# Optimization experiments

Measured on AMD Instinct MI355X. Metric: run time of the kernel, lower is better.

## Reference

```python
import jax, jax.numpy as jnp
import numpy as np

EPS = 1e-5

def group_norm(x, num_groups, eps=EPS):
    # x: [B, C, H, W]; no affine (matches F.group_norm with weight=None)
    B, C, H, W = x.shape
    xg = x.reshape(B, num_groups, (C // num_groups) * H * W)
    mean = jnp.mean(xg, axis=-1, keepdims=True)
    var = jnp.var(xg, axis=-1, keepdims=True)
    xg = (xg - mean) * jax.lax.rsqrt(var + eps)
    return xg.reshape(B, C, H, W)

def setup_inputs() -> dict:
    key = jax.random.key(0)
    ks = jax.random.split(key, 5)
    B, C, H, W = 32, 256, 32, 32
    # kaiming-uniform-ish scale for linear weights
    bound = 1.0 / np.sqrt(C)
    x = jax.random.normal(ks[0], (B, C, H, W), dtype=jnp.float32)
    WQ = jax.random.uniform(ks[1], (C, C), jnp.float32, -bound, bound)
    WK = jax.random.uniform(ks[2], (C, C), jnp.float32, -bound, bound)
    WV = jax.random.uniform(ks[3], (C, C), jnp.float32, -bound, bound)
    Wo = jax.random.uniform(ks[4], (C, C), jnp.float32, -bound, bound)
    z = jnp.zeros((C,), jnp.float32)
    return {"x": x, "WQ": WQ, "bQ": z, "WK": WK, "bK": z,
            "WV": WV, "bV": z, "Wo": Wo, "bo": z}

def reference(x, WQ, bQ, WK, bK, WV, bV, Wo, bo):
    B, C, H, W = x.shape
    G = min(32, C)
    h = group_norm(x, G)                      # [B,C,H,W]
    h = h.reshape(B, C, H * W).transpose(0, 2, 1)  # [B, S, C], S = H*W
    q = h @ WQ + bQ
    k = h @ WK + bK
    v = h @ WV + bV
    scale = C ** (-0.5)
    attn = jnp.einsum('bsc,btc->bst', q, k) * scale   # [B,S,S]
    attn = jax.nn.softmax(attn, axis=-1)
    o = jnp.einsum('bst,btc->bsc', attn, v)           # [B,S,C]
    o = o @ Wo + bo                                   # output Nin while in [B,S,C]
    o = o.transpose(0, 2, 1).reshape(B, C, H, W)
    return x + o
```

## Files before the change

kernel.cpp:

```cpp
#include <hip/hip_runtime.h>
#include <stdint.h>

#define BB  32
#define CC  256
#define SS  1024
#define GG  32
#define GCH 8
#define EPS 1e-5f

typedef __attribute__((ext_vector_type(8))) short short8;
typedef __attribute__((ext_vector_type(4))) float f32x4;
typedef unsigned short ushort;

__device__ __forceinline__ float bf2f(ushort u){
  union { unsigned int i; float f; } v; v.i = ((unsigned int)u) << 16; return v.f;
}
__device__ __forceinline__ ushort f2bf(float f){
  union { float f; unsigned int i; } v; v.f = f;
  unsigned int r = v.i + 0x7FFFu + ((v.i >> 16) & 1u);
  return (ushort)(r >> 16);
}

typedef __attribute__((address_space(3))) unsigned int lds_uint;
typedef const __attribute__((address_space(1))) unsigned int glob_uint;
__device__ __forceinline__ void ld_lds16(const void* g, void* l){
  __builtin_amdgcn_global_load_lds((glob_uint*)g, (lds_uint*)l, 16, 0, 0);
}

__global__ __launch_bounds__(256) void sniff_k(const unsigned int* __restrict__ xw,
                                               int* __restrict__ flag)
{
  const int tid = threadIdx.x;
  unsigned int w = xw[tid];
  ushort lo = (ushort)(w & 0xFFFFu);
  int e = (lo >> 7) & 0xFF;
  int ok = (lo == 0 || (e >= 100 && e <= 130)) ? 1 : 0;
  __shared__ int cnt;
  if (tid == 0) cnt = 0;
  __syncthreads();
  atomicAdd(&cnt, ok);
  __syncthreads();
  if (tid == 0) *flag = (cnt > 192) ? 1 : 0;
}

__global__ __launch_bounds__(256) void convert_pre(
    const void* w0, const void* w1, const void* w2, const void* w3,
    const void* b0, const void* b1, const void* b2, const void* b3,
    ushort* __restrict__ WT, float* __restrict__ biasF,
    const int* __restrict__ flag)
{
  const int f = *flag;
  const int z = blockIdx.z;
  const float scl = (z == 0) ? 0.0625f : 1.0f;
  const void* wsel = z==0?w0:z==1?w1:z==2?w2:w3;
  ushort* dst = WT + (long long)z * 65536;
  __shared__ ushort t[64][65];
  const int tid = threadIdx.x;
  const int tx = tid & 63, ty = tid >> 6;
  const int r0 = blockIdx.x * 64, c0 = blockIdx.y * 64;
  for (int j = 0; j < 64; j += 4){
    const int idx = (r0+ty+j)*256 + c0+tx;
    float v = f ? bf2f(((const ushort*)wsel)[idx]) : ((const float*)wsel)[idx];
    t[ty+j][tx] = f2bf(v * scl);
  }
  __syncthreads();
  for (int j = 0; j < 64; j += 4) dst[(c0+ty+j)*256 + r0+tx] = t[tx][ty+j];
  if (blockIdx.x == 0 && blockIdx.y == 0){
    const void* bsel = z==0?b0:z==1?b1:z==2?b2:b3;
    float bv = f ? bf2f(((const ushort*)bsel)[tid]) : ((const float*)bsel)[tid];
    biasF[z*256 + tid] = bv * scl;
  }
}

__global__ __launch_bounds__(256) void gn_stats(const void* __restrict__ x,
                                                float* __restrict__ stats,
                                                const int* __restrict__ flag)
{
  const int f = *flag;
  const int g = blockIdx.x, b = blockIdx.y;
  const int tid = threadIdx.x;
  const long long base = ((long long)b * CC + g * GCH) * SS;
  float sum = 0.f, ss = 0.f;
  if (f){
    const ushort* xg = (const ushort*)x + base;
    #pragma unroll
    for (int j = 0; j < 4; j++){
      uint4 u = *(const uint4*)(xg + (j*256 + tid)*8);
      const ushort* e = (const ushort*)&u;
      #pragma unroll
      for (int i = 0; i < 8; i++){ float v = bf2f(e[i]); sum += v; ss += v*v; }
    }
  } else {
    const float* xg = (const float*)x + base;
    #pragma unroll
    for (int j = 0; j < 8; j++){
      float4 v4 = *(const float4*)(xg + (j*256 + tid)*4);
      sum += v4.x+v4.y+v4.z+v4.w;
      ss  += v4.x*v4.x+v4.y*v4.y+v4.z*v4.z+v4.w*v4.w;
    }
  }
  __shared__ float red[8];
  const int lane = tid & 63, w = tid >> 6;
  #pragma unroll
  for (int o = 32; o > 0; o >>= 1){
    sum += __shfl_down(sum, o);
    ss  += __shfl_down(ss, o);
  }
  if (lane == 0){ red[w] = sum; red[4+w] = ss; }
  __syncthreads();
  if (tid == 0){
    float s1 = red[0]+red[1]+red[2]+red[3];
    float s2 = red[4]+red[5]+red[6]+red[7];
    float mean = s1 / (float)(GCH*SS);
    float var  = s2 / (float)(GCH*SS) - mean*mean;
    const int idx = b*GG + g;
    stats[idx*2]   = mean;
    stats[idx*2+1] = rsqrtf(var + EPS);
  }
}

__global__ __launch_bounds__(256) void gn_norm(const void* __restrict__ x,
                                               ushort* __restrict__ h,
                                               const float* __restrict__ stats,
                                               const int* __restrict__ flag)
{
  const int f = *flag;
  const int c0 = blockIdx.x * 64, s0 = blockIdx.y * 64, b = blockIdx.z;
  const int tid = threadIdx.x;
  __shared__ ushort T[64][72];
  const int row = tid >> 2;
  const int qr  = tid & 3;
  const int g = (c0 + row) >> 3;
  const float mean = stats[(b*GG + g)*2];
  const float rstd = stats[(b*GG + g)*2 + 1];
  const long long xrow = ((long long)b * CC + c0 + row) * SS + s0;
  if (f){
    const ushort* xr = (const ushort*)x + xrow;
    #pragma unroll
    for (int j = 0; j < 2; j++){
      const int col = qr*16 + j*8;
      uint4 u = *(const uint4*)(xr + col);
      const ushort* e = (const ushort*)&u;
      #pragma unroll
      for (int i = 0; i < 8; i++) T[row][col+i] = f2bf((bf2f(e[i]) - mean) * rstd);
    }
  } else {
    const float* xr = (const float*)x + xrow;
    #pragma unroll
    for (int j = 0; j < 4; j++){
      const int col = qr*16 + j*4;
      float4 v4 = *(const float4*)(xr + col);
      T[row][col+0] = f2bf((v4.x - mean) * rstd);
      T[row][col+1] = f2bf((v4.y - mean) * rstd);
      T[row][col+2] = f2bf((v4.z - mean) * rstd);
      T[row][col+3] = f2bf((v4.w - mean) * rstd);
    }
  }
  __syncthreads();
  #pragma unroll
  for (int pass = 0; pass < 2; pass++){
    const int sr = pass*32 + (tid >> 3);
    const int cl = (tid & 7) * 8;
    ushort tmp[8];
    #pragma unroll
    for (int e = 0; e < 8; e++) tmp[e] = T[cl+e][sr];
    *(uint4*)(&h[((long long)b * SS + s0 + sr) * CC + c0 + cl]) = *(const uint4*)tmp;
  }
}

template<int MODE>
__global__ __launch_bounds__(256) void gemm128(
    const ushort* __restrict__ A,
    const ushort* __restrict__ BT,
    ushort* __restrict__ Cmat,
    int lda, int ldb, int ldc, int K,
    long long sA, long long sB, long long sC,
    const float* __restrict__ biasF,
    const void* __restrict__ xres,
    void* __restrict__ outp,
    ushort* __restrict__ vTp,
    long long xoff,
    const int* __restrict__ flag)
{
  extern __shared__ __attribute__((aligned(16))) ushort smem[];
  ushort* As = smem;
  ushort* Bs = smem + 5120;
  const int tid  = threadIdx.x;
  const int lane = tid & 63;
  const int w    = tid >> 6;
  const int wr   = w >> 1, wc = w & 1;
  const int bz   = blockIdx.z;
  const int m0 = blockIdx.x * 128;
  const int n0 = blockIdx.y * 128;

  const int srow  = tid >> 1;
  const int shalf = (tid & 1) * 16;

  f32x4 acc[4][4] = {};

  const ushort* Ablk = A + (long long)bz * sA + (long long)(m0 + srow) * lda + shalf;
  const ushort* Bblk = BT + (long long)bz * sB + (long long)(n0 + srow) * ldb + shalf;
  ushort* asw = &As[srow * 40 + shalf];
  ushort* bsw = &Bs[srow * 40 + shalf];

  const int koff = 8 * (lane >> 4);
  const int rr   = lane & 15;

  for (int k0 = 0; k0 < K; k0 += 32){
    uint4 va0 = *(const uint4*)(Ablk + k0);
    uint4 va1 = *(const uint4*)(Ablk + k0 + 8);
    uint4 vb0 = *(const uint4*)(Bblk + k0);
    uint4 vb1 = *(const uint4*)(Bblk + k0 + 8);
    *(uint4*)(asw)     = va0;
    *(uint4*)(asw + 8) = va1;
    *(uint4*)(bsw)     = vb0;
    *(uint4*)(bsw + 8) = vb1;
    __syncthreads();
    short8 af[4], bfr[4];
    #pragma unroll
    for (int mf = 0; mf < 4; mf++)
      af[mf] = *(const short8*)(&As[(wr*64 + mf*16 + rr) * 40 + koff]);
    #pragma unroll
    for (int nf = 0; nf < 4; nf++)
      bfr[nf] = *(const short8*)(&Bs[(wc*64 + nf*16 + rr) * 40 + koff]);
    #pragma unroll
    for (int mf = 0; mf < 4; mf++)
      #pragma unroll
      for (int nf = 0; nf < 4; nf++)
        acc[mf][nf] = __builtin_amdgcn_mfma_f32_16x16x32_bf16(af[mf], bfr[nf], acc[mf][nf], 0, 0, 0);
    __syncthreads();
  }

  const int rb = 4 * (lane >> 4);
  if (MODE == 0){
    if (bz < 2){
      ushort* Co = Cmat + (long long)bz * sC;
      #pragma unroll
      for (int mf = 0; mf < 4; mf++){
        #pragma unroll
        for (int nf = 0; nf < 4; nf++){
          const int col = n0 + wc*64 + nf*16 + rr;
          const float badd = biasF[bz*256 + col];
          #pragma unroll
          for (int r = 0; r < 4; r++){
            const int row = m0 + wr*64 + mf*16 + rb + r;
            Co[(long long)row * ldc + col] = f2bf(acc[mf][nf][r] + badd);
          }
        }
      }
    } else {
      #pragma unroll
      for (int mf = 0; mf < 4; mf++){
        #pragma unroll
        for (int nf = 0; nf < 4; nf++){
          const int col = n0 + wc*64 + nf*16 + rr;
          const float badd = biasF[512 + col];
          #pragma unroll
          for (int r = 0; r < 4; r++){
            const int row = m0 + wr*64 + mf*16 + rb + r;
            const int bL = row >> 10, s = row & 1023;
            vTp[((long long)bL * CC + col) * SS + s] = f2bf(acc[mf][nf][r] + badd);
          }
        }
      }
    }
  } else {
    const int bL = m0 >> 10;
    const int s0 = m0 & 1023;
    #pragma unroll
    for (int mf = 0; mf < 4; mf++){
      #pragma unroll
      for (int nf = 0; nf < 4; nf++){
        const int colL = wc*64 + nf*16 + rr;
        const float badd = biasF[768 + n0 + colL];
        #pragma unroll
        for (int r = 0; r < 4; r++){
          const int rowL = wr*64 + mf*16 + rb + r;
          smem[colL * 128 + rowL] = f2bf(acc[mf][nf][r] + badd);
        }
      }
    }
    __syncthreads();
    const int f = *flag;
    for (int i = tid; i < 2048; i += 256){
      const int colL = i >> 4;
      const int rowL = (i & 15) * 8;
      const long long oi = xoff + ((long long)bL * CC + n0 + colL) * SS + s0 + rowL;
      const ushort* pu = &smem[colL * 128 + rowL];
      if (f){
        const ushort* xu = (const ushort*)xres + oi;
        ushort* ou = (ushort*)outp + oi;
        ushort tmp[8];
        #pragma unroll
        for (int e = 0; e < 8; e++) tmp[e] = f2bf(bf2f(xu[e]) + bf2f(pu[e]));
        *(uint4*)ou = *(const uint4*)tmp;
      } else {
        const float* xf = (const float*)xres + oi;
        float* of = (float*)outp + oi;
        float4 a0 = *(const float4*)xf;
        float4 a1 = *(const float4*)(xf + 4);
        float4 r0, r1;
        r0.x = a0.x + bf2f(pu[0]); r0.y = a0.y + bf2f(pu[1]);
        r0.z = a0.z + bf2f(pu[2]); r0.w = a0.w + bf2f(pu[3]);
        r1.x = a1.x + bf2f(pu[4]); r1.y = a1.y + bf2f(pu[5]);
        r1.z = a1.z + bf2f(pu[6]); r1.w = a1.w + bf2f(pu[7]);
        *(float4*)of = r0;
        *(float4*)(of + 4) = r1;
      }
    }
  }
}

__global__ __launch_bounds__(256, 2) void attn_fused(
    const ushort* __restrict__ q, const ushort* __restrict__ k,
    const ushort* __restrict__ vT, ushort* __restrict__ oC)
{
  __shared__ ushort Kb[64 * 256];
  __shared__ ushort Vb[256 * 64];
  __shared__ ushort Pb[64 * 64];
  const int tid = threadIdx.x, lane = tid & 63, w = tid >> 6;
  const int hi = lane >> 4, rr = lane & 15;
  const int b = blockIdx.x, qt = blockIdx.y;

  const ushort* qg = q + ((long long)b * SS + qt * 64) * CC;
  const char* kgB = (const char*)(k + (long long)b * SS * CC);
  const char* vgB = (const char*)(vT + (long long)b * CC * SS);
  ushort* og = oC + ((long long)b * SS + qt * 64) * CC;

  short8 qf[8];
  #pragma unroll
  for (int ks = 0; ks < 8; ks++)
    qf[ks] = *(const short8*)(qg + (w*16 + rr) * CC + ks*32 + 8*hi);

  f32x4 Oa[16] = {};
  float mrow[4], lrow[4];
  #pragma unroll
  for (int r = 0; r < 4; r++){ mrow[r] = -1e30f; lrow[r] = 0.0f; }

  for (int t0 = 0; t0 < SS; t0 += 64){
    #pragma unroll
    for (int j = 0; j < 8; j++){
      const int tr = j*8 + w*2 + (lane >> 5);
      const int xb = ((lane & 31) * 16) ^ ((tr & 7) << 4);
      ld_lds16(kgB + (long long)(t0 + tr) * 512 + xb, &Kb[(j*8 + w*2) * 256]);
    }
    #pragma unroll
    for (int j = 0; j < 8; j++){
      const int c0 = (j*4 + w) * 8;
      const int cr = c0 + (lane >> 3);
      const int yb = ((lane & 7) * 16) ^ ((cr & 7) << 4);
      ld_lds16(vgB + (long long)cr * 2048 + t0*2 + yb, &Vb[c0 * 64]);
    }
    asm volatile("s_waitcnt vmcnt(0)" ::: "memory");
    __builtin_amdgcn_sched_barrier(0);
    __syncthreads();

    f32x4 Sa[4] = {};
    __builtin_amdgcn_s_setprio(1);
    #pragma unroll
    for (int ks = 0; ks < 8; ks++){
      short8 bk[4];
      #pragma unroll
      for (int nf = 0; nf < 4; nf++){
        const int t = nf*16 + rr;
        const int byte = t*512 + ((ks*64 + hi*16) ^ ((t & 7) << 4));
        bk[nf] = *(const short8*)((const char*)Kb + byte);
      }
      #pragma unroll
      for (int nf = 0; nf < 4; nf++)
        Sa[nf] = __builtin_amdgcn_mfma_f32_16x16x32_bf16(qf[ks], bk[nf], Sa[nf], 0, 0, 0);
    }
    __builtin_amdgcn_s_setprio(0);

    #pragma unroll
    for (int r = 0; r < 4; r++){
      float pm = fmaxf(fmaxf(Sa[0][r], Sa[1][r]), fmaxf(Sa[2][r], Sa[3][r]));
      pm = fmaxf(pm, __shfl_xor(pm, 1));
      pm = fmaxf(pm, __shfl_xor(pm, 2));
      pm = fmaxf(pm, __shfl_xor(pm, 4));
      pm = fmaxf(pm, __shfl_xor(pm, 8));
      const float mo = mrow[r];
      const float mn = fmaxf(mo, pm);
      const float sc = __expf(mo - mn);
      float ps[4];
      #pragma unroll
      for (int nf = 0; nf < 4; nf++) ps[nf] = __expf(Sa[nf][r] - mn);
      float rs = ps[0] + ps[1] + ps[2] + ps[3];
      rs += __shfl_xor(rs, 1);
      rs += __shfl_xor(rs, 2);
      rs += __shfl_xor(rs, 4);
      rs += __shfl_xor(rs, 8);
      lrow[r] = lrow[r] * sc + rs;
      mrow[r] = mn;
      const int qloc = w*16 + 4*hi + r;
      const int swz = (qloc & 7) << 4;
      #pragma unroll
      for (int nf = 0; nf < 4; nf++){
        const int byte = qloc*128 + ((2*(nf*16 + rr)) ^ swz);
        *(ushort*)((char*)Pb + byte) = f2bf(ps[nf]);
      }
      #pragma unroll
      for (int nf2 = 0; nf2 < 16; nf2++) Oa[nf2][r] *= sc;
    }

    __builtin_amdgcn_s_setprio(1);
    #pragma unroll
    for (int ks2 = 0; ks2 < 2; ks2++){
      const int qloc = w*16 + rr;
      const int pbyte = qloc*128 + ((ks2*64 + 16*hi) ^ ((qloc & 7) << 4));
      short8 pa = *(const short8*)((const char*)Pb + pbyte);
      #pragma unroll
      for (int nf = 0; nf < 16; nf++){
        const int c = nf*16 + rr;
        const int byte = c*128 + ((ks2*64 + 16*hi) ^ ((c & 7) << 4));
        short8 bv = *(const short8*)((const char*)Vb + byte);
        Oa[nf] = __builtin_amdgcn_mfma_f32_16x16x32_bf16(pa, bv, Oa[nf], 0, 0, 0);
      }
    }
    __builtin_amdgcn_s_setprio(0);
    __syncthreads();
  }

  #pragma unroll
  for (int r = 0; r < 4; r++){
    const float inv = 1.0f / lrow[r];
    const int qloc = w*16 + 4*hi + r;
    #pragma unroll
    for (int nf = 0; nf < 16; nf++)
      og[(long long)qloc * CC + nf*16 + rr] = f2bf(Oa[nf][r] * inv);
  }
}

extern "C" void kernel_launch(void* const* d_in, const int* in_sizes, int n_in,
                              void* d_out, int out_size, void* d_ws, size_t ws_size,
                              hipStream_t stream)
{
  (void)in_sizes; (void)n_in; (void)out_size;
  const void* x  = d_in[0];
  const void* WQ = d_in[1];
  const void* bQ = d_in[2];
  const void* WK = d_in[3];
  const void* bK = d_in[4];
  const void* WV = d_in[5];
  const void* bV = d_in[6];
  const void* Wo = d_in[7];
  const void* bo = d_in[8];

  const long long NE  = (long long)BB * SS * CC;
  const long long SC  = (long long)SS * CC;

  uint8_t* base = (uint8_t*)d_ws;
  int* flag          = (int*)base;
  float* biasF       = (float*)(base + 256);
  float* stats       = (float*)(base + 256 + 4096);
  ushort* WT         = (ushort*)(base + 256 + 4096 + 8192);
  ushort* h          = WT + 4 * 65536;

  const long long fixedB = 256 + 4096 + 8192 + 4LL*65536*2 + NE*2;
  int CB = 1;
  for (int c = 32; c >= 1; c >>= 1){
    if (fixedB + 4LL * c * SC * 2 <= (long long)ws_size){ CB = c; break; }
  }

  ushort* q  = h + NE;
  ushort* k  = q + (long long)CB * SC;
  ushort* vT = k + (long long)CB * SC;
  ushort* oC = vT + (long long)CB * SC;

  dim3 blk(256);
  const size_t shmem = 32768;

  sniff_k<<<1, blk, 0, stream>>>((const unsigned int*)x, flag);
  convert_pre<<<dim3(4, 4, 4), blk, 0, stream>>>(WQ, WK, WV, Wo, bQ, bK, bV, bo, WT, biasF, flag);
  gn_stats<<<dim3(GG, BB), blk, 0, stream>>>(x, stats, flag);
  gn_norm<<<dim3(4, 16, BB), blk, 0, stream>>>(x, h, stats, flag);

  for (int c0 = 0; c0 < BB; c0 += CB){
    const ushort* hC = h + (long long)c0 * SC;
    gemm128<0><<<dim3(CB*8, 2, 3), blk, shmem, stream>>>(
        hC, WT, q, CC, CC, CC, CC,
        0LL, 65536LL, (long long)CB * SC,
        biasF, nullptr, nullptr, vT, 0LL, flag);
    attn_fused<<<dim3(CB, 16), blk, 0, stream>>>(q, k, vT, oC);
    gemm128<3><<<dim3(CB*8, 2, 1), blk, shmem, stream>>>(
        oC, WT + 3*65536, nullptr, CC, CC, SS, CC,
        0LL, 0LL, 0LL,
        biasF, x, d_out, nullptr, (long long)c0 * SC, flag);
  }
}
```

Before: 148.2 us.

## Rewrite attention kernel with 32x32 MFMA and direct global K/V loads

```diff
diff --git a/kernel.cpp b/kernel.cpp
--- a/kernel.cpp
+++ b/kernel.cpp
@@ -10,6 +10,7 @@
 
 typedef __attribute__((ext_vector_type(8))) short short8;
 typedef __attribute__((ext_vector_type(4))) float f32x4;
+typedef __attribute__((ext_vector_type(16))) float f32x16;
 typedef unsigned short ushort;
 
 __device__ __forceinline__ float bf2f(ushort u){
@@ -19,12 +20,6 @@
   union { float f; unsigned int i; } v; v.f = f;
   unsigned int r = v.i + 0x7FFFu + ((v.i >> 16) & 1u);
   return (ushort)(r >> 16);
-}
-
-typedef __attribute__((address_space(3))) unsigned int lds_uint;
-typedef const __attribute__((address_space(1))) unsigned int glob_uint;
-__device__ __forceinline__ void ld_lds16(const void* g, void* l){
-  __builtin_amdgcn_global_load_lds((glob_uint*)g, (lds_uint*)l, 16, 0, 0);
 }
 
 __global__ __launch_bounds__(256) void sniff_k(const unsigned int* __restrict__ xw,
@@ -315,119 +310,112 @@
     const ushort* __restrict__ q, const ushort* __restrict__ k,
     const ushort* __restrict__ vT, ushort* __restrict__ oC)
 {
-  __shared__ ushort Kb[64 * 256];
-  __shared__ ushort Vb[256 * 64];
-  __shared__ ushort Pb[64 * 64];
+  __shared__ ushort Pall[4][2048];
+  __shared__ float  Sall[4][32];
   const int tid = threadIdx.x, lane = tid & 63, w = tid >> 6;
-  const int hi = lane >> 4, rr = lane & 15;
-  const int b = blockIdx.x, qt = blockIdx.y;
-
-  const ushort* qg = q + ((long long)b * SS + qt * 64) * CC;
-  const char* kgB = (const char*)(k + (long long)b * SS * CC);
-  const char* vgB = (const char*)(vT + (long long)b * CC * SS);
-  ushort* og = oC + ((long long)b * SS + qt * 64) * CC;
-
-  short8 qf[8];
+  const int l31 = lane & 31, hi2 = lane >> 5;
+  const int qh = w & 1, ch = w >> 1;
+  const int qt = blockIdx.x, b = blockIdx.y;
+
+  const ushort* qg = q + ((long long)b * SS + qt*64 + qh*32 + l31) * CC + 8*hi2;
+  const ushort* kbase = k + (long long)b * SS * CC + (long long)l31 * CC + 8*hi2;
+  const ushort* vbase = vT + (long long)b * CC * SS + (long long)(ch*128 + l31) * SS + 8*hi2;
+  ushort* og = oC + ((long long)b * SS + qt*64 + qh*32) * CC + ch*128;
+
+  char* PwB = (char*)&Pall[w][0];
+  float* Sw = &Sall[w][0];
+  const int swz = (l31 & 7) << 4;
+
+  short8 qf[16];
   #pragma unroll
-  for (int ks = 0; ks < 8; ks++)
-    qf[ks] = *(const short8*)(qg + (w*16 + rr) * CC + ks*32 + 8*hi);
-
-  f32x4 Oa[16] = {};
-  float mrow[4], lrow[4];
+  for (int kk = 0; kk < 16; kk++)
+    qf[kk] = *(const short8*)(qg + kk*16);
+
+  f32x16 Oa[4] = {};
+  float mrow = -1e30f, lrow = 0.0f;
+
+  for (int t0 = 0; t0 < SS; t0 += 64){
+    const ushort* kt0 = kbase + (long long)t0 * CC;
+    const ushort* kt1 = kt0 + 32 * CC;
+
+    f32x16 Sa0 = {}, Sa1 = {};
+    __builtin_amdgcn_s_setprio(1);
+    #pragma unroll
+    for (int kk = 0; kk < 16; kk++){
+      short8 ka0 = *(const short8*)(kt0 + kk*16);
+      short8 ka1 = *(const short8*)(kt1 + kk*16);
+      Sa0 = __builtin_amdgcn_mfma_f32_32x32x16_bf16(ka0, qf[kk], Sa0, 0, 0, 0);
+      Sa1 = __builtin_amdgcn_mfma_f32_32x32x16_bf16(ka1, qf[kk], Sa1, 0, 0, 0);
+    }
+    __builtin_amdgcn_s_setprio(0);
+
+    float mx = -1e30f;
+    #pragma unroll
+    for (int r = 0; r < 16; r++){ mx = fmaxf(mx, Sa0[r]); mx = fmaxf(mx, Sa1[r]); }
+    mx = fmaxf(mx, __shfl_xor(mx, 32));
+    const float mn = fmaxf(mrow, mx);
+    const float sc = __expf(mrow - mn);
+    mrow = mn;
+    float rs = 0.0f;
+    #pragma unroll
+    for (int r = 0; r < 16; r++){
+      Sa0[r] = __expf(Sa0[r] - mn); rs += Sa0[r];
+      Sa1[r] = __expf(Sa1[r] - mn); rs += Sa1[r];
+    }
+    rs += __shfl_xor(rs, 32);
+    lrow = lrow * sc + rs;
+
+    if (hi2 == 0) Sw[l31] = sc;
+
+    #pragma unroll
+    for (int g2 = 0; g2 < 4; g2++){
+      ushort t4[4];
+      #pragma unroll
+      for (int j = 0; j < 4; j++) t4[j] = f2bf(Sa0[g2*4 + j]);
+      *(uint2*)(PwB + l31*128 + ((g2*16 + hi2*8) ^ swz)) = *(const uint2*)t4;
+      #pragma unroll
+      for (int j = 0; j < 4; j++) t4[j] = f2bf(Sa1[g2*4 + j]);
+      *(uint2*)(PwB + l31*128 + ((64 + g2*16 + hi2*8) ^ swz)) = *(const uint2*)t4;
+    }
+
+    f32x4 scv[4];
+    #pragma unroll
+    for (int g2 = 0; g2 < 4; g2++)
+      scv[g2] = *(const f32x4*)((const char*)Sw + g2*32 + hi2*16);
+    #pragma unroll
+    for (int nf = 0; nf < 4; nf++)
+      #pragma unroll
+      for (int r = 0; r < 16; r++)
+        Oa[nf][r] *= scv[r >> 2][r & 3];
+
+    __builtin_amdgcn_s_setprio(1);
+    #pragma unroll
+    for (int kk = 0; kk < 4; kk++){
+      short8 pa = *(const short8*)(PwB + l31*128 + ((kk*32 + hi2*16) ^ swz));
+      #pragma unroll
+      for (int nf = 0; nf < 4; nf++){
+        short8 bv = *(const short8*)(vbase + (long long)(nf*32) * SS + t0 + kk*16);
+        Oa[nf] = __builtin_amdgcn_mfma_f32_32x32x16_bf16(pa, bv, Oa[nf], 0, 0, 0);
+      }
+    }
+    __builtin_amdgcn_s_setprio(0);
+  }
+
+  if (hi2 == 0) Sw[l31] = 1.0f / lrow;
+  f32x4 iv[4];
   #pragma unroll
-  for (int r = 0; r < 4; r++){ mrow[r] = -1e30f; lrow[r] = 0.0f; }
-
-  for (int t0 = 0; t0 < SS; t0 += 64){
-    #pragma unroll
-    for (int j = 0; j < 8; j++){
-      const int tr = j*8 + w*2 + (lane >> 5);
-      const int xb = ((lane & 31) * 16) ^ ((tr & 7) << 4);
-      ld_lds16(kgB + (long long)(t0 + tr) * 512 + xb, &Kb[(j*8 + w*2) * 256]);
-    }
-    #pragma unroll
-    for (int j = 0; j < 8; j++){
-      const int c0 = (j*4 + w) * 8;
-      const int cr = c0 + (lane >> 3);
-      const int yb = ((lane & 7) * 16) ^ ((cr & 7) << 4);
-      ld_lds16(vgB + (long long)cr * 2048 + t0*2 + yb, &Vb[c0 * 64]);
-    }
-    asm volatile("s_waitcnt vmcnt(0)" ::: "memory");
-    __builtin_amdgcn_sched_barrier(0);
-    __syncthreads();
-
-    f32x4 Sa[4] = {};
-    __builtin_amdgcn_s_setprio(1);
-    #pragma unroll
-    for (int ks = 0; ks < 8; ks++){
-      short8 bk[4];
-      #pragma unroll
-      for (int nf = 0; nf < 4; nf++){
-        const int t = nf*16 + rr;
-        const int byte = t*512 + ((ks*64 + hi*16) ^ ((t & 7) << 4));
-        bk[nf] = *(const short8*)((const char*)Kb + byte);
-      }
-      #pragma unroll
-      for (int nf = 0; nf < 4; nf++)
-        Sa[nf] = __builtin_amdgcn_mfma_f32_16x16x32_bf16(qf[ks], bk[nf], Sa[nf], 0, 0, 0);
-    }
-    __builtin_amdgcn_s_setprio(0);
-
-    #pragma unroll
-    for (int r = 0; r < 4; r++){
-      float pm = fmaxf(fmaxf(Sa[0][r], Sa[1][r]), fmaxf(Sa[2][r], Sa[3][r]));
-      pm = fmaxf(pm, __shfl_xor(pm, 1));
-      pm = fmaxf(pm, __shfl_xor(pm, 2));
-      pm = fmaxf(pm, __shfl_xor(pm, 4));
-      pm = fmaxf(pm, __shfl_xor(pm, 8));
-      const float mo = mrow[r];
-      const float mn = fmaxf(mo, pm);
-      const float sc = __expf(mo - mn);
-      float ps[4];
-      #pragma unroll
-      for (int nf = 0; nf < 4; nf++) ps[nf] = __expf(Sa[nf][r] - mn);
-      float rs = ps[0] + ps[1] + ps[2] + ps[3];
-      rs += __shfl_xor(rs, 1);
-      rs += __shfl_xor(rs, 2);
-      rs += __shfl_xor(rs, 4);
-      rs += __shfl_xor(rs, 8);
-      lrow[r] = lrow[r] * sc + rs;
-      mrow[r] = mn;
-      const int qloc = w*16 + 4*hi + r;
-      const int swz = (qloc & 7) << 4;
-      #pragma unroll
-      for (int nf = 0; nf < 4; nf++){
-        const int byte = qloc*128 + ((2*(nf*16 + rr)) ^ swz);
-        *(ushort*)((char*)Pb + byte) = f2bf(ps[nf]);
-      }
-      #pragma unroll
-      for (int nf2 = 0; nf2 < 16; nf2++) Oa[nf2][r] *= sc;
-    }
-
-    __builtin_amdgcn_s_setprio(1);
-    #pragma unroll
-    for (int ks2 = 0; ks2 < 2; ks2++){
-      const int qloc = w*16 + rr;
-      const int pbyte = qloc*128 + ((ks2*64 + 16*hi) ^ ((qloc & 7) << 4));
-      short8 pa = *(const short8*)((const char*)Pb + pbyte);
-      #pragma unroll
-      for (int nf = 0; nf < 16; nf++){
-        const int c = nf*16 + rr;
-        const int byte = c*128 + ((ks2*64 + 16*hi) ^ ((c & 7) << 4));
-        short8 bv = *(const short8*)((const char*)Vb + byte);
-        Oa[nf] = __builtin_amdgcn_mfma_f32_16x16x32_bf16(pa, bv, Oa[nf], 0, 0, 0);
-      }
-    }
-    __builtin_amdgcn_s_setprio(0);
-    __syncthreads();
-  }
-
+  for (int g2 = 0; g2 < 4; g2++)
+    iv[g2] = *(const f32x4*)((const char*)Sw + g2*32 + hi2*16);
   #pragma unroll
-  for (int r = 0; r < 4; r++){
-    const float inv = 1.0f / lrow[r];
-    const int qloc = w*16 + 4*hi + r;
-    #pragma unroll
-    for (int nf = 0; nf < 16; nf++)
-      og[(long long)qloc * CC + nf*16 + rr] = f2bf(Oa[nf][r] * inv);
+  for (int nf = 0; nf < 4; nf++){
+    #pragma unroll
+    for (int g2 = 0; g2 < 4; g2++){
+      #pragma unroll
+      for (int j = 0; j < 4; j++){
+        const int rq = g2*8 + 4*hi2 + j;
+        og[(long long)rq * CC + nf*32 + l31] = f2bf(Oa[nf][g2*4 + j] * iv[g2][j]);
+      }
+    }
   }
 }
 
@@ -481,7 +469,7 @@
         hC, WT, q, CC, CC, CC, CC,
         0LL, 65536LL, (long long)CB * SC,
         biasF, nullptr, nullptr, vT, 0LL, flag);
-    attn_fused<<<dim3(CB, 16), blk, 0, stream>>>(q, k, vT, oC);
+    attn_fused<<<dim3(16, CB), blk, 0, stream>>>(q, k, vT, oC);
     gemm128<3><<<dim3(CB*8, 2, 1), blk, shmem, stream>>>(
         oC, WT + 3*65536, nullptr, CC, CC, SS, CC,
         0LL, 0LL, 0LL,
```

After: 267.8 us. 80.8% more time.
